# Performance work log

Measured on AMD Instinct MI355X. Metric: run time of the kernel, lower is better.

The kernel has to match this reference:

```python
import jax, jax.numpy as jnp
import numpy as np

HIDDEN = 768
VOCAB = 30522
PAD_IDX = 0


def setup_inputs() -> dict:
    key = jax.random.key(0)
    ks = jax.random.split(key, 12)
    B, J, X, D, V, K = 32, 4, 256, HIDDEN, VOCAB, 8
    s = 0.02
    return {
        "decoder_input": jax.random.normal(ks[0], (B, J, D), jnp.float32),
        "hidden": jax.random.normal(ks[1], (1, B, D), jnp.float32),
        "encoder_output": jax.random.normal(ks[2], (B, X, D), jnp.float32),
        "input_ids": jax.random.randint(ks[3], (B, X), 0, V),
        "max_len": K,
        "emb": jax.random.normal(ks[4], (V, D), jnp.float32) * s,
        "w_ih": jax.random.normal(ks[5], (3 * D, D), jnp.float32) * s,
        "w_hh": jax.random.normal(ks[6], (3 * D, D), jnp.float32) * s,
        "b_ih": jnp.zeros((3 * D,), jnp.float32),
        "b_hh": jnp.zeros((3 * D,), jnp.float32),
        "w_gen": jax.random.normal(ks[7], (1, 3 * D), jnp.float32) * s,
        "b_gen": jnp.zeros((1,), jnp.float32),
    }


def _gru_cell(x, h, w_ih, w_hh, b_ih, b_hh):
    # PyTorch GRUCell math. x,h: (B,D)
    gi = x @ w_ih.T + b_ih  # (B,3D)
    gh = h @ w_hh.T + b_hh
    i_r, i_z, i_n = jnp.split(gi, 3, axis=-1)
    h_r, h_z, h_n = jnp.split(gh, 3, axis=-1)
    r = jax.nn.sigmoid(i_r + h_r)
    z = jax.nn.sigmoid(i_z + h_z)
    n = jnp.tanh(i_n + r * h_n)
    return (1.0 - z) * n + z * h


def _decode(decoder_input, hidden, encoder_output, input_ids, max_len,
            emb, w_ih, w_hh, b_ih, b_hh, w_gen, b_gen):
    B = input_ids.shape[0]
    V = emb.shape[0]
    mask = input_ids == PAD_IDX  # (B,X)
    rows = jnp.arange(B)[:, None]
    h0 = hidden[0]  # (B,D)

    def step(carry, _):
        x, h = carry  # (B,D), (B,D)
        h = _gru_cell(x, h, w_ih, w_hh, b_ih, b_hh)
        # vocab distribution
        p_vcb = jax.nn.softmax(h @ emb.T, axis=-1)  # (B,V)
        # context attention
        attn_ctx = jnp.einsum("bxd,bd->bx", encoder_output, h)
        attn_ctx = jnp.where(mask, -1e9, attn_ctx)
        attn_ctx = jax.nn.softmax(attn_ctx, axis=-1)  # (B,X)
        context = jnp.einsum("bx,bxd->bd", attn_ctx, encoder_output)
        # pointer-generator gate
        p_gen = jax.nn.sigmoid(
            jnp.concatenate([h, x, context], axis=-1) @ w_gen.T + b_gen
        )  # (B,1)
        # scatter copy probs into vocab space
        p_ctx = jnp.zeros((B, V), attn_ctx.dtype).at[rows, input_ids].add(attn_ctx)
        p_svg = p_gen * p_vcb + (1.0 - p_gen) * p_ctx  # (B,V)
        x_next = emb[jnp.argmax(p_svg, axis=-1)]  # greedy next input (B,D)
        return (x_next, h), p_svg

    outs = []
    h = h0
    for j in range(decoder_input.shape[1]):  # small fixed J'
        (_, h), p = jax.lax.scan(step, (decoder_input[:, j, :], h), None,
                                 length=max_len)
        outs.append(jnp.transpose(p, (1, 0, 2)))  # (B,K,V)
    return jnp.stack(outs, axis=1)  # (B,J',K,V)


def reference(decoder_input, hidden, encoder_output, input_ids, max_len,
              emb, w_ih, w_hh, b_ih, b_hh, w_gen, b_gen):
    return _decode(decoder_input, hidden, encoder_output, input_ids, max_len,
                   emb, w_ih, w_hh, b_ih, b_hh, w_gen, b_gen)
```

## Files before the change

kernel.cpp:

```cpp
#include <hip/hip_runtime.h>
#include <hip/hip_bf16.h>

#define D 768
#define BB 32
#define XX 256
#define CH 3816

typedef __bf16 bf16x8 __attribute__((ext_vector_type(8)));
typedef float  f32x4  __attribute__((ext_vector_type(4)));

__global__ __launch_bounds__(256) void k_cvt(const float* __restrict__ src,
                                             __bf16* __restrict__ dst, int n8)
{
    int i = blockIdx.x * 256 + threadIdx.x;
    if (i < n8) {
        float4 f0 = *(const float4*)(src + (size_t)i * 8);
        float4 f1 = *(const float4*)(src + (size_t)i * 8 + 4);
        bf16x8 o;
        o[0] = (__bf16)f0.x; o[1] = (__bf16)f0.y; o[2] = (__bf16)f0.z; o[3] = (__bf16)f0.w;
        o[4] = (__bf16)f1.x; o[5] = (__bf16)f1.y; o[6] = (__bf16)f1.z; o[7] = (__bf16)f1.w;
        *(bf16x8*)(dst + (size_t)i * 8) = o;
    }
}

__global__ __launch_bounds__(256) void k_penc(
    const float* __restrict__ enc, const float* __restrict__ wgen,
    float* __restrict__ penc)
{
    const int t = threadIdx.x;
    const int b = blockIdx.x >> 2, c = blockIdx.x & 3;
    const int x0 = c * 64;
    const int l = t & 31;
    float4 wr[6];
    #pragma unroll
    for (int p = 0; p < 6; ++p)
        wr[p] = *(const float4*)(wgen + 1536 + l * 4 + p * 128);
    for (int g = 0; g < 8; ++g) {
        int x = x0 + g * 8 + (t >> 5);
        const float* er = enc + ((size_t)b * XX + x) * D + l * 4;
        float acc = 0.f;
        #pragma unroll
        for (int p = 0; p < 6; ++p) {
            float4 e = *(const float4*)(er + p * 128);
            acc += e.x * wr[p].x + e.y * wr[p].y + e.z * wr[p].z + e.w * wr[p].w;
        }
        #pragma unroll
        for (int m = 1; m <= 16; m <<= 1) acc += __shfl_xor(acc, m);
        if (l == 0) penc[b * XX + x] = acc;
    }
}

__global__ __launch_bounds__(256) void k_gates(
    const float* __restrict__ xbase, long xbstride,
    const unsigned long long* __restrict__ toks,
    const float* __restrict__ hin,
    const float* __restrict__ wih, const float* __restrict__ whh,
    float* __restrict__ gT)
{
    __shared__ __align__(16) float vec[BB][132];
    __shared__ int tokl[BB];
    const int t = threadIdx.x, bid = blockIdx.x;
    const int b = t & 31, rl = t >> 5;
    const int rglob = bid * 8 + rl;
    const bool isH = rglob >= 2304;
    const int row = isH ? rglob - 2304 : rglob;
    const float* w = (isH ? whh : wih) + (size_t)row * D;
    if (t < 32) tokl[t] = toks ? (int)(0xFFFFFFFFu - (unsigned)(toks[t] & 0xFFFFFFFFull)) : 0;

    float acc = 0.f;
    for (int c = 0; c < 6; ++c) {
        const int kc = c * 128;
        __syncthreads();
        for (int p = 0; p < 4; ++p) {
            int fid = t + 256 * p;
            int bb = fid >> 5, k4 = (fid & 31) * 4;
            const float* src;
            if (isH) src = hin + (size_t)bb * D;
            else     src = toks ? (xbase + (size_t)tokl[bb] * D)
                                : (xbase + (size_t)bb * xbstride);
            *(float4*)&vec[bb][k4] = *(const float4*)(src + kc + k4);
        }
        __syncthreads();
        #pragma unroll
        for (int k4 = 0; k4 < 128; k4 += 4) {
            float4 wv = *(const float4*)(w + kc + k4);
            float4 xv = *(const float4*)&vec[b][k4];
            acc += wv.x * xv.x + wv.y * xv.y + wv.z * xv.z + wv.w * xv.w;
        }
    }
    gT[(size_t)rglob * 32 + b] = acc;
}

__global__ __launch_bounds__(256) void k_comb(
    const float* __restrict__ gT,
    const float* __restrict__ bih, const float* __restrict__ bhh,
    const float* __restrict__ hin,
    const float* __restrict__ xbase, long xbstride,
    const unsigned long long* __restrict__ toks,
    const float* __restrict__ wgen,
    float* __restrict__ hout, __bf16* __restrict__ hbf,
    float* __restrict__ pgen_part,
    unsigned long long* __restrict__ argz)
{
    __shared__ float part[8][32];
    const int t = threadIdx.x, bid = blockIdx.x;
    const int b = t & 31, dl = t >> 5;
    const int d = bid * 8 + dl;
    if (bid == 0 && t < 32) argz[t] = 0ULL;
    float ir = gT[(size_t)d * 32 + b]            + bih[d];
    float iz = gT[(size_t)(768 + d) * 32 + b]    + bih[768 + d];
    float in_ = gT[(size_t)(1536 + d) * 32 + b]  + bih[1536 + d];
    float hr = gT[(size_t)(2304 + d) * 32 + b]   + bhh[d];
    float hz = gT[(size_t)(3072 + d) * 32 + b]   + bhh[768 + d];
    float hn = gT[(size_t)(3840 + d) * 32 + b]   + bhh[1536 + d];
    float r = 1.0f / (1.0f + expf(-(ir + hr)));
    float z = 1.0f / (1.0f + expf(-(iz + hz)));
    float n = tanhf(in_ + r * hn);
    float hold = hin[(size_t)b * D + d];
    float hv = (1.0f - z) * n + z * hold;
    hout[(size_t)b * D + d] = hv;
    hbf[(size_t)b * D + d] = (__bf16)hv;
    float xv;
    if (toks) {
        int tok = (int)(0xFFFFFFFFu - (unsigned)(toks[b] & 0xFFFFFFFFull));
        xv = xbase[(size_t)tok * D + d];
    } else {
        xv = xbase[(size_t)b * xbstride + d];
    }
    part[dl][b] = wgen[d] * hv + wgen[768 + d] * xv;
    __syncthreads();
    if (t < 32) {
        float s = 0.f;
        #pragma unroll
        for (int i = 0; i < 8; ++i) s += part[i][t];
        pgen_part[(size_t)t * 96 + bid] = s;
    }
}

__global__ __launch_bounds__(256) void k_mid(
    const float* __restrict__ hnew, const __bf16* __restrict__ hbf,
    const __bf16* __restrict__ embbf,
    const float* __restrict__ enc, const int* __restrict__ ids,
    float* __restrict__ out, long outoff, long JKV,
    float* __restrict__ dpartT, float* __restrict__ logitw,
    int V, int NVB)
{
    __shared__ float dsum[32];
    const int t = threadIdx.x;
    const int bid = blockIdx.x;

    if (bid < NVB) {
        if (t < 32) dsum[t] = 0.f;
        __syncthreads();

        const int lane = t & 63, w = t >> 6;
        const int col = lane & 15;
        const int kq  = (lane >> 4) * 8;
        int vrow = bid * 64 + w * 16 + col;
        const bool ok = vrow < V;
        const int vl = ok ? vrow : V - 1;
        const __bf16* bp  = embbf + (size_t)vl * D + kq;
        const __bf16* ap0 = hbf + (size_t)col * D + kq;
        const __bf16* ap1 = hbf + (size_t)(col + 16) * D + kq;

        f32x4 c0 = {0.f, 0.f, 0.f, 0.f};
        f32x4 c1 = {0.f, 0.f, 0.f, 0.f};
        #pragma unroll 4
        for (int kc = 0; kc < D; kc += 32) {
            bf16x8 bv = *(const bf16x8*)(bp + kc);
            bf16x8 a0 = *(const bf16x8*)(ap0 + kc);
            bf16x8 a1 = *(const bf16x8*)(ap1 + kc);
            c0 = __builtin_amdgcn_mfma_f32_16x16x32_bf16(a0, bv, c0, 0, 0, 0);
            c1 = __builtin_amdgcn_mfma_f32_16x16x32_bf16(a1, bv, c1, 0, 0, 0);
        }
        #pragma unroll
        for (int r = 0; r < 4; ++r) {
            int b0 = (lane >> 4) * 4 + r;
            float e0 = ok ? __expf(c0[r]) : 0.f;
            float e1 = ok ? __expf(c1[r]) : 0.f;
            if (ok) {
                out[(size_t)b0 * JKV + outoff + vrow] = e0;
                out[(size_t)(b0 + 16) * JKV + outoff + vrow] = e1;
            }
            #pragma unroll
            for (int m = 1; m <= 8; m <<= 1) {
                e0 += __shfl_xor(e0, m);
                e1 += __shfl_xor(e1, m);
            }
            if (col == 0) {
                atomicAdd(&dsum[b0], e0);
                atomicAdd(&dsum[b0 + 16], e1);
            }
        }
        __syncthreads();
        if (t < 32) dpartT[(size_t)t * 512 + bid] = dsum[t];
    } else {
        const int nb = bid - NVB;
        const int b = nb >> 2, c = nb & 3;
        const int x0 = c * 64;
        const int l = t & 31;
        float4 hr[6];
        #pragma unroll
        for (int p = 0; p < 6; ++p)
            hr[p] = *(const float4*)(hnew + (size_t)b * D + l * 4 + p * 128);
        for (int g = 0; g < 8; ++g) {
            int x = x0 + g * 8 + (t >> 5);
            const float* er = enc + ((size_t)b * XX + x) * D + l * 4;
            float acc = 0.f;
            #pragma unroll
            for (int p = 0; p < 6; ++p) {
                float4 e = *(const float4*)(er + p * 128);
                acc += e.x * hr[p].x + e.y * hr[p].y + e.z * hr[p].z + e.w * hr[p].w;
            }
            #pragma unroll
            for (int m = 1; m <= 16; m <<= 1) acc += __shfl_xor(acc, m);
            if (l == 0) {
                int id = ids[b * XX + x];
                logitw[b * XX + x] = (id == 0) ? -1e9f : acc;
            }
        }
    }
}

__global__ __launch_bounds__(256) void k_fin(
    float* __restrict__ out, long outoff, long JKV,
    const float* __restrict__ dpartT, int npart,
    const float* __restrict__ logitw, const float* __restrict__ penc,
    const float* __restrict__ pgen_part, const float* __restrict__ bgen,
    const int* __restrict__ ids,
    unsigned long long* __restrict__ argz, int V)
{
    __shared__ float pctx[CH];
    __shared__ float red[256];
    __shared__ float aw[256];
    __shared__ unsigned long long wmax[4];
    const int t = threadIdx.x;
    const int b = blockIdx.x >> 3;
    const int c = blockIdx.x & 7;
    const int v0 = c * CH;

    float s = 0.f;
    for (int i = t; i < npart; i += 256) s += dpartT[(size_t)b * 512 + i];
    red[t] = s;
    __syncthreads();
    for (int st = 128; st > 0; st >>= 1) {
        if (t < st) red[t] += red[t + st];
        __syncthreads();
    }
    const float rd = 1.0f / red[0];
    __syncthreads();

    float l = logitw[b * XX + t];
    red[t] = l;
    __syncthreads();
    for (int st = 128; st > 0; st >>= 1) {
        if (t < st) red[t] = fmaxf(red[t], red[t + st]);
        __syncthreads();
    }
    float mx = red[0];
    __syncthreads();
    float e = expf(l - mx);
    red[t] = e;
    __syncthreads();
    for (int st = 128; st > 0; st >>= 1) {
        if (t < st) red[t] += red[t + st];
        __syncthreads();
    }
    float awv = e / red[0];
    aw[t] = awv;
    __syncthreads();

    float pv = awv * penc[b * XX + t] + ((t < 96) ? pgen_part[(size_t)b * 96 + t] : 0.f);
    red[t] = pv;
    __syncthreads();
    for (int st = 128; st > 0; st >>= 1) {
        if (t < st) red[t] += red[t + st];
        __syncthreads();
    }
    const float pg = 1.0f / (1.0f + expf(-(red[0] + bgen[0])));
    const float og = 1.0f - pg;

    for (int i = t; i < CH; i += 256) pctx[i] = 0.f;
    __syncthreads();
    {
        int id = ids[b * XX + t];
        int rel = id - v0;
        if ((unsigned)rel < (unsigned)CH) atomicAdd(&pctx[rel], aw[t]);
    }
    __syncthreads();

    unsigned long long pk = 0ULL;
    const int vend = (v0 + CH < V) ? CH : (V - v0);
    #pragma unroll
    for (int i = 0; i < 15; ++i) {
        int v = t + 256 * i;
        if (v < vend) {
            int vg = v0 + v;
            size_t o = (size_t)b * JKV + outoff + vg;
            float ev = out[o];
            float ps = pg * ev * rd + og * pctx[v];
            out[o] = ps;
            unsigned long long k2 = ((unsigned long long)__float_as_uint(ps) << 32)
                                  | (unsigned long long)(0xFFFFFFFFu - (unsigned)vg);
            if (k2 > pk) pk = k2;
        }
    }
    #pragma unroll
    for (int m = 1; m < 64; m <<= 1) {
        unsigned long long o2 = __shfl_xor(pk, m);
        if (o2 > pk) pk = o2;
    }
    if ((t & 63) == 0) wmax[t >> 6] = pk;
    __syncthreads();
    if (t == 0) {
        unsigned long long m0 = wmax[0];
        #pragma unroll
        for (int i2 = 1; i2 < 4; ++i2) if (wmax[i2] > m0) m0 = wmax[i2];
        atomicMax(&argz[b], m0);
    }
}

extern "C" void kernel_launch(void* const* d_in, const int* in_sizes, int n_in,
                              void* d_out, int out_size, void* d_ws, size_t ws_size,
                              hipStream_t stream)
{
    const float* dec  = (const float*)d_in[0];
    const float* hid  = (const float*)d_in[1];
    const float* enc  = (const float*)d_in[2];
    const int*   ids  = (const int*)d_in[3];
    const float* emb  = (const float*)d_in[5];
    const float* wih  = (const float*)d_in[6];
    const float* whh  = (const float*)d_in[7];
    const float* bih  = (const float*)d_in[8];
    const float* bhh  = (const float*)d_in[9];
    const float* wgen = (const float*)d_in[10];
    const float* bgen = (const float*)d_in[11];
    float* out = (float*)d_out;

    const int B = 32;
    const int J = in_sizes[0] / (B * D);
    const int V = in_sizes[5] / D;
    const int K = out_size / (B * J * V);
    const long JKV = (long)J * K * V;
    const int NVB = (V + 63) / 64;
    const int NLG = 128;

    char* w = (char*)d_ws;
    unsigned long long* argpack = (unsigned long long*)w; w += 1024;
    float* gT        = (float*)w;  w += (size_t)4608 * 32 * 4;
    float* dpartT    = (float*)w;  w += (size_t)32 * 512 * 4;
    float* logitw    = (float*)w;  w += (size_t)B * XX * 4;
    float* penc      = (float*)w;  w += (size_t)B * XX * 4;
    float* pgen_part = (float*)w;  w += (size_t)B * 96 * 4;
    float* h0        = (float*)w;  w += (size_t)B * D * 4;
    float* h1        = (float*)w;  w += (size_t)B * D * 4;
    __bf16* hbf      = (__bf16*)w; w += (size_t)B * D * 2;
    __bf16* embbf    = (__bf16*)w; w += (size_t)V * D * 2;

    const int n8 = V * D / 8;
    k_cvt<<<dim3((n8 + 255) / 256), dim3(256), 0, stream>>>(emb, embbf, n8);
    k_penc<<<dim3(128), dim3(256), 0, stream>>>(enc, wgen, penc);

    int step = 0;
    for (int j = 0; j < J; ++j) {
        for (int kk = 0; kk < K; ++kk) {
            const int cur = step & 1;
            float* hout = (cur == 0) ? h0 : h1;
            const float* hin = (step == 0) ? hid : ((((step - 1) & 1) == 0) ? h0 : h1);
            const float* xbase;
            long xbs;
            const unsigned long long* toks;
            if (kk == 0) {
                xbase = dec + (size_t)j * D;
                xbs = (long)J * D;
                toks = nullptr;
            } else {
                xbase = emb;
                xbs = D;
                toks = argpack + ((step - 1) & 1) * 32;
            }
            unsigned long long* argz = argpack + cur * 32;
            const long outoff = (long)(j * K + kk) * V;

            k_gates<<<dim3(576), dim3(256), 0, stream>>>(
                xbase, xbs, toks, hin, wih, whh, gT);
            k_comb<<<dim3(96), dim3(256), 0, stream>>>(
                gT, bih, bhh, hin, xbase, xbs, toks, wgen, hout, hbf,
                pgen_part, argz);
            k_mid<<<dim3(NVB + NLG), dim3(256), 0, stream>>>(
                hout, hbf, embbf, enc, ids, out, outoff, JKV,
                dpartT, logitw, V, NVB);
            k_fin<<<dim3(256), dim3(256), 0, stream>>>(
                out, outoff, JKV, dpartT, NVB, logitw, penc, pgen_part,
                bgen, ids, argz, V);
            ++step;
        }
    }
}
```

Measured before the change: 2.339 ms.

## Reorder k_mid blocks, preload embedding rows, coalesce exp stores via LDS

Attention-logit blocks now take the low block indices so they are scheduled first, and vocab blocks follow. Each vocab block loads its whole embedding row slice (24 bf16x8 vectors) into registers before running the MFMA chain, giving more memory-level parallelism. The exp results are staged in a padded shared array so the output writes go out as contiguous 64-element runs per batch row instead of scattered 16-wide strided stores. The cost is higher register pressure from the preloaded vectors, which could lower occupancy, plus an extra LDS round trip.

```diff
diff --git a/kernel.cpp b/kernel.cpp
--- a/kernel.cpp
+++ b/kernel.cpp
@@ -5,6 +5,7 @@
 #define BB 32
 #define XX 256
 #define CH 3816
+#define NLG 128
 
 typedef __bf16 bf16x8 __attribute__((ext_vector_type(8)));
 typedef float  f32x4  __attribute__((ext_vector_type(4)));
@@ -146,56 +147,12 @@
     int V, int NVB)
 {
     __shared__ float dsum[32];
+    __shared__ float sh[64][33];
     const int t = threadIdx.x;
     const int bid = blockIdx.x;
 
-    if (bid < NVB) {
-        if (t < 32) dsum[t] = 0.f;
-        __syncthreads();
-
-        const int lane = t & 63, w = t >> 6;
-        const int col = lane & 15;
-        const int kq  = (lane >> 4) * 8;
-        int vrow = bid * 64 + w * 16 + col;
-        const bool ok = vrow < V;
-        const int vl = ok ? vrow : V - 1;
-        const __bf16* bp  = embbf + (size_t)vl * D + kq;
-        const __bf16* ap0 = hbf + (size_t)col * D + kq;
-        const __bf16* ap1 = hbf + (size_t)(col + 16) * D + kq;
-
-        f32x4 c0 = {0.f, 0.f, 0.f, 0.f};
-        f32x4 c1 = {0.f, 0.f, 0.f, 0.f};
-        #pragma unroll 4
-        for (int kc = 0; kc < D; kc += 32) {
-            bf16x8 bv = *(const bf16x8*)(bp + kc);
-            bf16x8 a0 = *(const bf16x8*)(ap0 + kc);
-            bf16x8 a1 = *(const bf16x8*)(ap1 + kc);
-            c0 = __builtin_amdgcn_mfma_f32_16x16x32_bf16(a0, bv, c0, 0, 0, 0);
-            c1 = __builtin_amdgcn_mfma_f32_16x16x32_bf16(a1, bv, c1, 0, 0, 0);
-        }
-        #pragma unroll
-        for (int r = 0; r < 4; ++r) {
-            int b0 = (lane >> 4) * 4 + r;
-            float e0 = ok ? __expf(c0[r]) : 0.f;
-            float e1 = ok ? __expf(c1[r]) : 0.f;
-            if (ok) {
-                out[(size_t)b0 * JKV + outoff + vrow] = e0;
-                out[(size_t)(b0 + 16) * JKV + outoff + vrow] = e1;
-            }
-            #pragma unroll
-            for (int m = 1; m <= 8; m <<= 1) {
-                e0 += __shfl_xor(e0, m);
-                e1 += __shfl_xor(e1, m);
-            }
-            if (col == 0) {
-                atomicAdd(&dsum[b0], e0);
-                atomicAdd(&dsum[b0 + 16], e1);
-            }
-        }
-        __syncthreads();
-        if (t < 32) dpartT[(size_t)t * 512 + bid] = dsum[t];
-    } else {
-        const int nb = bid - NVB;
+    if (bid < NLG) {
+        const int nb = bid;
         const int b = nb >> 2, c = nb & 3;
         const int x0 = c * 64;
         const int l = t & 31;
@@ -203,6 +160,7 @@
         #pragma unroll
         for (int p = 0; p < 6; ++p)
             hr[p] = *(const float4*)(hnew + (size_t)b * D + l * 4 + p * 128);
+        #pragma unroll 4
         for (int g = 0; g < 8; ++g) {
             int x = x0 + g * 8 + (t >> 5);
             const float* er = enc + ((size_t)b * XX + x) * D + l * 4;
@@ -217,6 +175,66 @@
             if (l == 0) {
                 int id = ids[b * XX + x];
                 logitw[b * XX + x] = (id == 0) ? -1e9f : acc;
+            }
+        }
+    } else {
+        const int vb = bid - NLG;
+        if (t < 32) dsum[t] = 0.f;
+        __syncthreads();
+
+        const int lane = t & 63, w = t >> 6;
+        const int col = lane & 15;
+        const int kq  = (lane >> 4) * 8;
+        int vrow = vb * 64 + w * 16 + col;
+        const bool ok = vrow < V;
+        const int vl = ok ? vrow : V - 1;
+        const __bf16* bp  = embbf + (size_t)vl * D + kq;
+        const __bf16* ap0 = hbf + (size_t)col * D + kq;
+        const __bf16* ap1 = hbf + (size_t)(col + 16) * D + kq;
+
+        bf16x8 bv[24];
+        #pragma unroll
+        for (int i = 0; i < 24; ++i)
+            bv[i] = *(const bf16x8*)(bp + i * 32);
+
+        f32x4 c0 = {0.f, 0.f, 0.f, 0.f};
+        f32x4 c1 = {0.f, 0.f, 0.f, 0.f};
+        #pragma unroll
+        for (int i = 0; i < 24; ++i) {
+            bf16x8 a0 = *(const bf16x8*)(ap0 + i * 32);
+            bf16x8 a1 = *(const bf16x8*)(ap1 + i * 32);
+            c0 = __builtin_amdgcn_mfma_f32_16x16x32_bf16(a0, bv[i], c0, 0, 0, 0);
+            c1 = __builtin_amdgcn_mfma_f32_16x16x32_bf16(a1, bv[i], c1, 0, 0, 0);
+        }
+
+        const int vloc = w * 16 + col;
+        #pragma unroll
+        for (int r = 0; r < 4; ++r) {
+            int b0 = (lane >> 4) * 4 + r;
+            float e0 = ok ? __expf(c0[r]) : 0.f;
+            float e1 = ok ? __expf(c1[r]) : 0.f;
+            sh[vloc][b0]      = e0;
+            sh[vloc][b0 + 16] = e1;
+            #pragma unroll
+            for (int m = 1; m <= 8; m <<= 1) {
+                e0 += __shfl_xor(e0, m);
+                e1 += __shfl_xor(e1, m);
+            }
+            if (col == 0) {
+                atomicAdd(&dsum[b0], e0);
+                atomicAdd(&dsum[b0 + 16], e1);
+            }
+        }
+        __syncthreads();
+        if (t < 32) dpartT[(size_t)t * 512 + vb] = dsum[t];
+
+        const int li = lane;
+        const int vg = vb * 64 + li;
+        if (vg < V) {
+            #pragma unroll
+            for (int i = 0; i < 8; ++i) {
+                int bb2 = w * 8 + i;
+                out[(size_t)bb2 * JKV + outoff + vg] = sh[li][bb2];
             }
         }
     }
@@ -343,7 +361,6 @@
     const int K = out_size / (B * J * V);
     const long JKV = (long)J * K * V;
     const int NVB = (V + 63) / 64;
-    const int NLG = 128;
 
     char* w = (char*)d_ws;
     unsigned long long* argpack = (unsigned long long*)w; w += 1024;
```

Result: no change. 2.333 ms (-0.3%).
